# Kernel tuning notes

Measured on AMD Instinct MI355X. Metric: run time of the kernel, lower is better.

The kernel has to match this reference:

```python
import math
import jax, jax.numpy as jnp
import numpy as np

N, C, H, Wsp = 128, 512, 28, 28
NCLS = 1000

def setup_inputs() -> dict:
    key = jax.random.key(0)
    k1, k2, k3 = jax.random.split(key, 3)
    feat = jax.random.normal(k1, (N, C, H, Wsp), dtype=jnp.float32)
    y = jax.random.randint(k2, (N,), 0, NCLS, dtype=jnp.int64)
    w = jax.random.normal(k3, (NCLS, C), dtype=jnp.float32) * 0.02  # Linear weight
    b = jnp.zeros((NCLS,), dtype=jnp.float32)                        # Linear bias
    return {"feat": feat, "y": y, "w": w, "b": b}

def reference(feat, y, w, b):
    # Probe(feat): global avg pool -> flatten -> linear
    pooled = feat.mean(axis=(2, 3))            # (N, C)
    pred_cas = pooled @ w.T + b                # (N, NCLS)
    # _get_mask_with_graph (training branch, y given).
    # logits(scores) = (scores * pooled_detached) @ w.T + b, so
    # d sum_n logits[n, y_n] / d scores[n, c] = w[y_n, c] * pooled[n, c] (closed form of autograd.grad).
    pooled_sg = jax.lax.stop_gradient(pooled)  # feat.detach() in original
    g = w[y] * pooled_sg                       # (N, C) grad wrt scores
    norm = jnp.linalg.norm(g, axis=1, keepdims=True)  # (N, 1)
    c = feat.shape[1]
    mask = 1.0 + g / norm * (math.sqrt(c) / 2.0)      # scores(=1) + normalized grad
    mask = jax.nn.softmax(mask, axis=1)        # (N, C)
    masked_feat = feat * mask[:, :, None, None]
    return masked_feat, pred_cas
```

## Files before the change

### kernel.cpp

```cpp
#include <hip/hip_runtime.h>
#include <math.h>

#define NB   128
#define CCH  512
#define HW   784
#define NCLS 1000
#define TOT4 12845056

typedef float f32x4 __attribute__((ext_vector_type(4)));

__global__ __launch_bounds__(256) void k_pool(const float* __restrict__ feat,
                                              float* __restrict__ pooled) {
    int wv = threadIdx.x >> 6, lane = threadIdx.x & 63;
    int ch = blockIdx.x * 4 + wv;
    const float* src = feat + (size_t)ch * HW;
    float s = 0.f;
#pragma unroll
    for (int it = 0; it < 3; ++it) {
        f32x4 v = *reinterpret_cast<const f32x4*>(src + it * 256 + lane * 4);
        s += v.x + v.y + v.z + v.w;
    }
    if (lane < 4) {
        f32x4 v = *reinterpret_cast<const f32x4*>(src + 768 + lane * 4);
        s += v.x + v.y + v.z + v.w;
    }
#pragma unroll
    for (int o = 32; o; o >>= 1) s += __shfl_down(s, o, 64);
    if (lane == 0) pooled[ch] = s * (1.0f / 784.0f);
}

#define LIN_BLOCKS 4000
__global__ __launch_bounds__(256) void k_head(const float* __restrict__ pooled,
                                              const float* __restrict__ w,
                                              const float* __restrict__ b,
                                              const int* __restrict__ y,
                                              float* __restrict__ pred,
                                              float* __restrict__ mask) {
    __shared__ float sp[4096];
    int t = threadIdx.x, lane = t & 63, wv = t >> 6;

    if (blockIdx.x < LIN_BLOCKS) {
        int cb = blockIdx.x % 250;
        int nb = blockIdx.x / 250;
        const float* pbase = pooled + (size_t)nb * 8 * CCH;
#pragma unroll
        for (int k = 0; k < 4; ++k)
            *reinterpret_cast<f32x4*>(sp + k * 1024 + t * 4) =
                *reinterpret_cast<const f32x4*>(pbase + k * 1024 + t * 4);
        __syncthreads();

        int cls = cb * 4 + wv;
        const float* wr = w + (size_t)cls * CCH;
        f32x4 a0 = *reinterpret_cast<const f32x4*>(wr + lane * 8);
        f32x4 a1 = *reinterpret_cast<const f32x4*>(wr + lane * 8 + 4);
        float bias = b[cls];
        float s[8];
#pragma unroll
        for (int nn = 0; nn < 8; ++nn) {
            f32x4 p0 = *reinterpret_cast<const f32x4*>(sp + nn * CCH + lane * 8);
            f32x4 p1 = *reinterpret_cast<const f32x4*>(sp + nn * CCH + lane * 8 + 4);
            s[nn] = a0.x * p0.x + a0.y * p0.y + a0.z * p0.z + a0.w * p0.w
                  + a1.x * p1.x + a1.y * p1.y + a1.z * p1.z + a1.w * p1.w;
        }
#pragma unroll
        for (int nn = 0; nn < 8; ++nn) {
            float v = s[nn];
#pragma unroll
            for (int o = 32; o; o >>= 1) v += __shfl_down(v, o, 64);
            if (lane == 0) pred[(size_t)(nb * 8 + nn) * NCLS + cls] = v + bias;
        }
    } else {
        int n = blockIdx.x - LIN_BLOCKS;
        int cls = y[n];
        const float* wr = w + (size_t)cls * CCH;
        const float* pr = pooled + (size_t)n * CCH;
        float g0 = wr[t] * pr[t];
        float g1 = wr[t + 256] * pr[t + 256];

        float ss = g0 * g0 + g1 * g1;
#pragma unroll
        for (int o = 32; o; o >>= 1) ss += __shfl_down(ss, o, 64);
        if (lane == 0) sp[wv] = ss;
        __syncthreads();
        if (t == 0) sp[8] = sqrtf(sp[0] + sp[1] + sp[2] + sp[3]);
        __syncthreads();
        float inv = 11.313708498984761f / sp[8];
        float v0 = 1.0f + g0 * inv, v1 = 1.0f + g1 * inv;
        __syncthreads();

        float mx = fmaxf(v0, v1);
#pragma unroll
        for (int o = 32; o; o >>= 1) mx = fmaxf(mx, __shfl_down(mx, o, 64));
        if (lane == 0) sp[wv] = mx;
        __syncthreads();
        if (t == 0) sp[8] = fmaxf(fmaxf(sp[0], sp[1]), fmaxf(sp[2], sp[3]));
        __syncthreads();
        float m = sp[8];
        float e0 = expf(v0 - m), e1 = expf(v1 - m);
        __syncthreads();

        float se = e0 + e1;
#pragma unroll
        for (int o = 32; o; o >>= 1) se += __shfl_down(se, o, 64);
        if (lane == 0) sp[wv] = se;
        __syncthreads();
        if (t == 0) sp[8] = sp[0] + sp[1] + sp[2] + sp[3];
        __syncthreads();
        float is = 1.0f / sp[8];
        mask[(size_t)n * CCH + t] = e0 * is;
        mask[(size_t)n * CCH + t + 256] = e1 * is;
    }
}

__global__ __launch_bounds__(256) void k_apply(const float* __restrict__ feat,
                                               const float* __restrict__ mask,
                                               float* __restrict__ out) {
    unsigned int i = blockIdx.x * 256u + threadIdx.x;
    unsigned int ch = i / 196u;
    float m = mask[ch];
    f32x4 v = reinterpret_cast<const f32x4*>(feat)[i];
    v.x *= m; v.y *= m; v.z *= m; v.w *= m;
    __builtin_nontemporal_store(v, reinterpret_cast<f32x4*>(out) + i);
}

extern "C" void kernel_launch(void* const* d_in, const int* in_sizes, int n_in,
                              void* d_out, int out_size, void* d_ws, size_t ws_size,
                              hipStream_t stream) {
    const float* feat = (const float*)d_in[0];
    const int*   y    = (const int*)d_in[1];
    const float* w    = (const float*)d_in[2];
    const float* b    = (const float*)d_in[3];

    float* out_feat = (float*)d_out;
    float* out_pred = out_feat + (size_t)NB * CCH * HW;

    float* pooled = (float*)d_ws;
    float* maskp  = pooled + NB * CCH;

    k_pool <<<(NB * CCH) / 4, 256, 0, stream>>>(feat, pooled);
    k_head <<<LIN_BLOCKS + NB, 256, 0, stream>>>(pooled, w, b, y, out_pred, maskp);
    k_apply<<<TOT4 / 256, 256, 0, stream>>>(feat, maskp, out_feat);
}
```

Before: 106.1 us.

## Pipeline pooling and mask-apply across batch groups in a fused kernel

Splits the batch into four groups of 32 and launches a fused kernel that applies the mask to the previous group while pooling the next group, with a per-group head kernel in between. The aim is to keep feat for the most recent group in the large last-level cache between the pool read and the apply read, and to overlap the head's latency with streaming work. In exchange it issues nine launches instead of three, and each launch boundary is a serialization point that adds tail and launch overhead.

```diff
diff --git a/kernel.cpp b/kernel.cpp
--- a/kernel.cpp
+++ b/kernel.cpp
@@ -1,48 +1,70 @@
 #include <hip/hip_runtime.h>
 #include <math.h>
 
-#define NB   128
-#define CCH  512
-#define HW   784
-#define NCLS 1000
-#define TOT4 12845056
+#define NB    128
+#define CCH   512
+#define HW    784
+#define NCLS  1000
+#define GRP   32
+#define NGRP  4
+#define PCHG  16384
+#define ABLK  12544
+#define PBLK  4096
 
 typedef float f32x4 __attribute__((ext_vector_type(4)));
 
-__global__ __launch_bounds__(256) void k_pool(const float* __restrict__ feat,
-                                              float* __restrict__ pooled) {
-    int wv = threadIdx.x >> 6, lane = threadIdx.x & 63;
-    int ch = blockIdx.x * 4 + wv;
-    const float* src = feat + (size_t)ch * HW;
-    float s = 0.f;
+__global__ __launch_bounds__(256) void k_fused(const float* __restrict__ feat,
+                                               float* __restrict__ pooled,
+                                               const float* __restrict__ mask,
+                                               float* __restrict__ out,
+                                               int g, int aBlk) {
+    int t = threadIdx.x;
+    if ((int)blockIdx.x < aBlk) {
+        int go = g - 1;
+        unsigned int i = blockIdx.x * 256u + t;
+        unsigned int chl = i / 196u;
+        float m = mask[go * PCHG + chl];
+        size_t gi = (size_t)go * (GRP * CCH * 196) + i;
+        f32x4 v = reinterpret_cast<const f32x4*>(feat)[gi];
+        v.x *= m; v.y *= m; v.z *= m; v.w *= m;
+        __builtin_nontemporal_store(v, reinterpret_cast<f32x4*>(out) + gi);
+    } else {
+        int wv = t >> 6, lane = t & 63;
+        int chl = ((int)blockIdx.x - aBlk) * 4 + wv;
+        int ch = g * PCHG + chl;
+        const float* src = feat + (size_t)ch * HW;
+        float s = 0.f;
 #pragma unroll
-    for (int it = 0; it < 3; ++it) {
-        f32x4 v = *reinterpret_cast<const f32x4*>(src + it * 256 + lane * 4);
-        s += v.x + v.y + v.z + v.w;
+        for (int it = 0; it < 3; ++it) {
+            f32x4 v = *reinterpret_cast<const f32x4*>(src + it * 256 + lane * 4);
+            s += v.x + v.y + v.z + v.w;
+        }
+        if (lane < 4) {
+            f32x4 v = *reinterpret_cast<const f32x4*>(src + 768 + lane * 4);
+            s += v.x + v.y + v.z + v.w;
+        }
+#pragma unroll
+        for (int o = 32; o; o >>= 1) s += __shfl_down(s, o, 64);
+        if (lane == 0) pooled[ch] = s * (1.0f / 784.0f);
     }
-    if (lane < 4) {
-        f32x4 v = *reinterpret_cast<const f32x4*>(src + 768 + lane * 4);
-        s += v.x + v.y + v.z + v.w;
-    }
-#pragma unroll
-    for (int o = 32; o; o >>= 1) s += __shfl_down(s, o, 64);
-    if (lane == 0) pooled[ch] = s * (1.0f / 784.0f);
 }
 
-#define LIN_BLOCKS 4000
+#define LINB 1000
 __global__ __launch_bounds__(256) void k_head(const float* __restrict__ pooled,
                                               const float* __restrict__ w,
                                               const float* __restrict__ b,
                                               const int* __restrict__ y,
                                               float* __restrict__ pred,
-                                              float* __restrict__ mask) {
+                                              float* __restrict__ mask,
+                                              int g) {
     __shared__ float sp[4096];
     int t = threadIdx.x, lane = t & 63, wv = t >> 6;
 
-    if (blockIdx.x < LIN_BLOCKS) {
+    if (blockIdx.x < LINB) {
         int cb = blockIdx.x % 250;
         int nb = blockIdx.x / 250;
-        const float* pbase = pooled + (size_t)nb * 8 * CCH;
+        int n0 = g * GRP + nb * 8;
+        const float* pbase = pooled + (size_t)n0 * CCH;
 #pragma unroll
         for (int k = 0; k < 4; ++k)
             *reinterpret_cast<f32x4*>(sp + k * 1024 + t * 4) =
@@ -67,10 +89,10 @@
             float v = s[nn];
 #pragma unroll
             for (int o = 32; o; o >>= 1) v += __shfl_down(v, o, 64);
-            if (lane == 0) pred[(size_t)(nb * 8 + nn) * NCLS + cls] = v + bias;
+            if (lane == 0) pred[(size_t)(n0 + nn) * NCLS + cls] = v + bias;
         }
     } else {
-        int n = blockIdx.x - LIN_BLOCKS;
+        int n = g * GRP + ((int)blockIdx.x - LINB);
         int cls = y[n];
         const float* wr = w + (size_t)cls * CCH;
         const float* pr = pooled + (size_t)n * CCH;
@@ -112,17 +134,6 @@
     }
 }
 
-__global__ __launch_bounds__(256) void k_apply(const float* __restrict__ feat,
-                                               const float* __restrict__ mask,
-                                               float* __restrict__ out) {
-    unsigned int i = blockIdx.x * 256u + threadIdx.x;
-    unsigned int ch = i / 196u;
-    float m = mask[ch];
-    f32x4 v = reinterpret_cast<const f32x4*>(feat)[i];
-    v.x *= m; v.y *= m; v.z *= m; v.w *= m;
-    __builtin_nontemporal_store(v, reinterpret_cast<f32x4*>(out) + i);
-}
-
 extern "C" void kernel_launch(void* const* d_in, const int* in_sizes, int n_in,
                               void* d_out, int out_size, void* d_ws, size_t ws_size,
                               hipStream_t stream) {
@@ -137,7 +148,11 @@
     float* pooled = (float*)d_ws;
     float* maskp  = pooled + NB * CCH;
 
-    k_pool <<<(NB * CCH) / 4, 256, 0, stream>>>(feat, pooled);
-    k_head <<<LIN_BLOCKS + NB, 256, 0, stream>>>(pooled, w, b, y, out_pred, maskp);
-    k_apply<<<TOT4 / 256, 256, 0, stream>>>(feat, maskp, out_feat);
+    for (int g = 0; g <= NGRP; ++g) {
+        int aBlk = (g >= 1) ? ABLK : 0;
+        int pBlk = (g < NGRP) ? PBLK : 0;
+        k_fused<<<aBlk + pBlk, 256, 0, stream>>>(feat, pooled, maskp, out_feat, g, aBlk);
+        if (g < NGRP)
+            k_head<<<LINB + GRP, 256, 0, stream>>>(pooled, w, b, y, out_pred, maskp, g);
+    }
 }
```

Result: slower. 125.3 us (+18.2%).
